# Kernel optimization log

Hardware: AMD Instinct MI355X
Metric: run time of the kernel (lower is better)

## Reference

```python
import jax, jax.numpy as jnp
import numpy as np

B, T, IN, H, LAYERS = 32, 512, 512, 512, 2


def _lstm_dir(x, Wx, Wh, b, reverse):
    """AugmentedLstm with highway, one direction.
    x: (B,T,I), Wx: (I,6H), Wh: (H,5H), b: (5H). Returns (B,T,H), h_final, c_final."""
    h = Wh.shape[0]
    # precompute input projections for all timesteps: (T,B,6H)
    px = jnp.einsum('bti,ig->tbg', x, Wx)
    if reverse:
        px = px[::-1]
    bsz = x.shape[0]
    h0 = jnp.zeros((bsz, h), x.dtype)
    c0 = jnp.zeros((bsz, h), x.dtype)

    def step(carry, pxt):
        hp, cp = carry
        ps = hp @ Wh + b  # (B,5H)
        i = jax.nn.sigmoid(pxt[:, 0*h:1*h] + ps[:, 0*h:1*h])
        f = jax.nn.sigmoid(pxt[:, 1*h:2*h] + ps[:, 1*h:2*h])
        g = jnp.tanh(pxt[:, 2*h:3*h] + ps[:, 2*h:3*h])
        o = jax.nn.sigmoid(pxt[:, 3*h:4*h] + ps[:, 3*h:4*h])
        c = i * g + f * cp
        ht = o * jnp.tanh(c)
        # highway: gate*h_t + (1-gate)*(W_x2 x_t)
        r = jax.nn.sigmoid(pxt[:, 4*h:5*h] + ps[:, 4*h:5*h])
        ht = r * ht + (1.0 - r) * pxt[:, 5*h:6*h]
        return (ht, c), ht

    (hf, cf), ys = jax.lax.scan(step, (h0, c0), px)
    if reverse:
        ys = ys[::-1]
    return jnp.transpose(ys, (1, 0, 2)), hf, cf


def setup_inputs() -> dict:
    key = jax.random.key(0)
    ks = jax.random.split(key, 16)
    d = {'x': jax.random.normal(ks[0], (B, T, IN), jnp.float32)}
    in_sizes = [IN, 2 * H]
    i = 1
    for l in range(LAYERS):
        isz = in_sizes[l]
        for dname in ('f', 'b'):
            d[f'Wx{l}{dname}'] = jax.random.normal(ks[i], (isz, 6 * H), jnp.float32) / np.sqrt(isz); i += 1
            d[f'Wh{l}{dname}'] = jax.random.normal(ks[i], (H, 5 * H), jnp.float32) / np.sqrt(H); i += 1
            d[f'b{l}{dname}'] = jnp.zeros((5 * H,), jnp.float32)
    return d


def reference(x, Wx0f, Wh0f, b0f, Wx0b, Wh0b, b0b,
              Wx1f, Wh1f, b1f, Wx1b, Wh1b, b1b):
    params = [((Wx0f, Wh0f, b0f), (Wx0b, Wh0b, b0b)),
              ((Wx1f, Wh1f, b1f), (Wx1b, Wh1b, b1b))]
    out = x
    final_h, final_c = [], []
    for (pf, pb) in params:
        yf, hf, cf = _lstm_dir(out, *pf, reverse=False)
        yb, hb, cb = _lstm_dir(out, *pb, reverse=True)
        out = jnp.concatenate([yf, yb], axis=-1)  # (B,T,2H)
        final_h.append(jnp.concatenate([hf, hb], axis=-1)[None])  # (1,B,2H)
        final_c.append(jnp.concatenate([cf, cb], axis=-1)[None])
    # torch code cats per-layer (1,B,2H) states along dim=1 -> (1, layers*B, 2H)
    final_h = jnp.concatenate(final_h, axis=1)
    final_c = jnp.concatenate(final_c, axis=1)
    return out, final_h, final_c
```

## Files before the change

### kernel.cpp

```cpp
#include <hip/hip_runtime.h>


typedef float f32x4 __attribute__((ext_vector_type(4)));
typedef __bf16 bf16x8 __attribute__((ext_vector_type(8)));
typedef unsigned short us8 __attribute__((ext_vector_type(8)));
typedef unsigned short us4 __attribute__((ext_vector_type(4)));
typedef unsigned int u32x4 __attribute__((ext_vector_type(4)));

__device__ __forceinline__ unsigned short f2bf(float f) {
  unsigned int u = __float_as_uint(f);
  u += 0x7FFFu + ((u >> 16) & 1u);
  return (unsigned short)(u >> 16);
}
__device__ __forceinline__ float bf2f(unsigned short h) {
  return __uint_as_float(((unsigned int)h) << 16);
}
__device__ __forceinline__ float sigf(float x) { return 1.0f / (1.0f + __expf(-x)); }
__device__ __forceinline__ float tanh_(float x) { return 2.0f / (1.0f + __expf(-2.0f * x)) - 1.0f; }

#define MFMA(a, b, c) __builtin_amdgcn_mfma_f32_16x16x32_bf16((a), (b), (c), 0, 0, 0)
#define GLOAD_LDS(gp, lp)                                                           \
  __builtin_amdgcn_global_load_lds(                                                 \
      (const __attribute__((address_space(1))) void*)(gp),                          \
      (__attribute__((address_space(3))) void*)(lp), 16, 0, 0)

__device__ __forceinline__ void chunk2_load(const char* p, u32x4& a, u32x4& b) {
  asm volatile(
      "global_load_dwordx4 %0, %2, off sc0 sc1\n\t"
      "global_load_dwordx4 %1, %2, off offset:16 sc0 sc1"
      : "=&v"(a), "=&v"(b) : "v"(p) : "memory");
}
__device__ __forceinline__ void hstore16(char* p, u32x4 v) {
  asm volatile("global_store_dwordx4 %0, %1, off sc0 sc1" :: "v"(p), "v"(v) : "memory");
}


__global__ void k_convert_x(const float* __restrict__ x, unsigned short* __restrict__ xb, int n4) {
  int i = blockIdx.x * blockDim.x + threadIdx.x;
  if (i < n4) {
    float4 v = ((const float4*)x)[i];
    us4 o;
    o[0] = f2bf(v.x); o[1] = f2bf(v.y); o[2] = f2bf(v.z); o[3] = f2bf(v.w);
    ((us4*)xb)[i] = o;
  }
}

__global__ __launch_bounds__(256) void k_pack_wxT(
    const float* __restrict__ W0, const float* __restrict__ W1,
    const float* __restrict__ W2, const float* __restrict__ W3,
    unsigned short* __restrict__ o01, unsigned short* __restrict__ o23) {
  int y = blockIdx.z;
  int K = (y >> 1) ? 1024 : 512;
  int kb = blockIdx.y * 32;
  if (kb >= K) return;
  const float* W = (y == 0) ? W0 : (y == 1) ? W1 : (y == 2) ? W2 : W3;
  unsigned short* o = (y >> 1) ? (o23 + (size_t)(y & 1) * 3072 * 1024)
                               : (o01 + (size_t)(y & 1) * 3072 * 512);
  __shared__ float tile[32][33];
  int nb = blockIdx.x * 32;
  int tx = threadIdx.x & 31, ty = threadIdx.x >> 5;
#pragma unroll
  for (int r = 0; r < 4; ++r)
    tile[ty + r * 8][tx] = W[(size_t)(kb + ty + r * 8) * 3072 + nb + tx];
  __syncthreads();
#pragma unroll
  for (int r = 0; r < 4; ++r)
    o[(size_t)(nb + ty + r * 8) * K + kb + tx] = f2bf(tile[tx][ty + r * 8]);
}

__global__ void k_pack_whp(const float* __restrict__ W0, const float* __restrict__ W1,
                           const float* __restrict__ W2, const float* __restrict__ W3,
                           unsigned short* __restrict__ out) {
  int y = blockIdx.y;
  const float* W = (y == 0) ? W0 : (y == 1) ? W1 : (y == 2) ? W2 : W3;
  unsigned short* o = out + (size_t)y * 1310720;
  int v = blockIdx.x * 256 + threadIdx.x;
  int lane = v & 63, ks = (v >> 6) & 15, ns = (v >> 10) & 31, g = v >> 15;
  int col = g * 512 + ns * 16 + (lane & 15);
  int kb = ks * 32 + ((lane >> 4) << 3);
  us8 vec;
#pragma unroll
  for (int e = 0; e < 8; ++e) vec[e] = f2bf(W[(size_t)(kb + e) * 2560 + col]);
  *(us8*)&o[(size_t)v * 8] = vec;
}

__global__ __launch_bounds__(256) void k_gemm(const unsigned short* __restrict__ A,
                                              const unsigned short* __restrict__ BtBase,
                                              unsigned short* __restrict__ CBase, int K) {
  __shared__ __align__(128) unsigned short As[128 * 32];
  __shared__ __align__(128) unsigned short Bs[128 * 32];
  const unsigned short* Bt = BtBase + (size_t)blockIdx.z * 3072 * K;
  unsigned short* C = CBase + (size_t)blockIdx.z * 16384 * 3072;
  int tid = threadIdx.x;
  int w = tid >> 6, l = tid & 63;
  int m0 = blockIdx.x * 128, n0 = blockIdx.y * 128;
  int wr = (w >> 1) * 64, wc = (w & 1) * 64;
  f32x4 acc[4][4];
#pragma unroll
  for (int i = 0; i < 4; ++i)
#pragma unroll
    for (int j = 0; j < 4; ++j) acc[i][j] = (f32x4){0.f, 0.f, 0.f, 0.f};

  for (int k0 = 0; k0 < K; k0 += 32) {
    __syncthreads();
#pragma unroll
    for (int half = 0; half < 2; ++half) {
      int r = w * 32 + half * 16 + (l >> 2);
      int gq = (l & 3) ^ (r & 3);
      GLOAD_LDS(A + (size_t)(m0 + r) * K + k0 + gq * 8, &As[(w * 32 + half * 16) * 32]);
      GLOAD_LDS(Bt + (size_t)(n0 + r) * K + k0 + gq * 8, &Bs[(w * 32 + half * 16) * 32]);
    }
    __syncthreads();
    bf16x8 af[4], bfr[4];
#pragma unroll
    for (int mi = 0; mi < 4; ++mi) {
      int r = wr + mi * 16 + (l & 15);
      int q = (l >> 4) ^ (r & 3);
      af[mi] = __builtin_bit_cast(bf16x8, *(const us8*)&As[r * 32 + q * 8]);
    }
#pragma unroll
    for (int ni = 0; ni < 4; ++ni) {
      int r = wc + ni * 16 + (l & 15);
      int q = (l >> 4) ^ (r & 3);
      bfr[ni] = __builtin_bit_cast(bf16x8, *(const us8*)&Bs[r * 32 + q * 8]);
    }
#pragma unroll
    for (int mi = 0; mi < 4; ++mi)
#pragma unroll
      for (int ni = 0; ni < 4; ++ni) acc[mi][ni] = MFMA(af[mi], bfr[ni], acc[mi][ni]);
  }
#pragma unroll
  for (int mi = 0; mi < 4; ++mi)
#pragma unroll
    for (int ni = 0; ni < 4; ++ni)
#pragma unroll
      for (int r4 = 0; r4 < 4; ++r4) {
        int row = m0 + wr + mi * 16 + (l >> 4) * 4 + r4;
        int rr = ((row & 511) << 5) + (row >> 9);
        int col = n0 + wc + ni * 16 + (l & 15);
        C[(size_t)rr * 3072 + col] = f2bf(acc[mi][ni][r4]);
      }
}

__global__ __launch_bounds__(256, 1) void k_persist(
    const unsigned short* __restrict__ px,
    const unsigned short* __restrict__ wp,
    const float* __restrict__ bias_f, const float* __restrict__ bias_b,
    char* __restrict__ hxc,
    unsigned short* __restrict__ ybf,
    float* __restrict__ yf,
    float* __restrict__ finals,
    int layer) {
  __shared__ float part[4][8][80];
  int wg = blockIdx.x;
  int grp = wg >> 4, m = wg & 15;
  int d = grp & 1, q = grp >> 1;
  int tid = threadIdx.x;
  int w = tid >> 6, l = tid & 63;
  int kh = w >> 1, nh = w & 1;
  int ns = m * 2 + nh;
  const unsigned short* wpd = wp + (size_t)d * 1310720;
  const unsigned short* pxd = px + (size_t)d * 16384 * 3072;
  const float* bias = d ? bias_b : bias_f;

  bf16x8 wf[5][8];
#pragma unroll
  for (int g5 = 0; g5 < 5; ++g5)
#pragma unroll
    for (int kk = 0; kk < 8; ++kk)
      wf[g5][kk] = __builtin_bit_cast(
          bf16x8,
          *(const us8*)&wpd[(size_t)((g5 * 32 + ns) * 16 + kh * 8 + kk) * 512 + l * 8]);

  int r = tid >> 5, j = tid & 31, jg = m * 32 + j, b = q * 8 + r;
  float bv[5];
#pragma unroll
  for (int g5 = 0; g5 < 5; ++g5) bv[g5] = bias[(g5 << 9) + jg];

  float c = 0.f;
  unsigned short xv[6];
  {
    int t0 = d ? 511 : 0;
    const unsigned short* pp = pxd + ((size_t)((t0 << 5) + b)) * 3072 + jg;
#pragma unroll
    for (int q6 = 0; q6 < 6; ++q6) xv[q6] = pp[q6 << 9];
  }

  int sel = l >> 4;
  int p0 = (sel == 1) ? 1 : (sel == 2) ? 2 : (sel == 3) ? 4 : 0;
  bool s1 = (sel == 1), s2 = (sel == 2);
  int lrow = l & 15;
  int row8 = l & 7;
  char* hxg = hxc + (size_t)grp * 12288;
  int coff[8];
#pragma unroll
  for (int kk = 0; kk < 8; ++kk)
    coff[kk] = (((kh * 8 + kk) * 8 + row8) * 6 + p0) * 16;
  int myc = l & 31;
  int pbase = l & 32;
  int prow = 2 * w + (l >> 5);

  for (int s = 0; s < 512; ++s) {
    int t = d ? (511 - s) : s;
    char* cbase = hxg + (size_t)(s & 1) * 98304;

    u32x4 ca[8], cb2[8];
    {
      unsigned int tgt = (unsigned int)s;
      long guard = 0;
      bool ok;
      do {
        if (lrow < 8) {
#pragma unroll
          for (int kk = 0; kk < 8; ++kk)
            chunk2_load(cbase + coff[kk], ca[kk], cb2[kk]);
        }
        asm volatile("s_waitcnt vmcnt(0)" ::: "memory");
        bool mine = true;
        if (lrow < 8) {
#pragma unroll
          for (int kk = 0; kk < 8; ++kk)
            mine = mine && (ca[kk][3] == tgt) && (cb2[kk][3] == tgt);
        }
        ok = (__all((int)mine) != 0);
      } while (!ok && ++guard < 50000);
    }

    f32x4 acc[5];
#pragma unroll
    for (int g5 = 0; g5 < 5; ++g5) acc[g5] = (f32x4){0.f, 0.f, 0.f, 0.f};
#pragma unroll
    for (int kk = 0; kk < 8; ++kk) {
      u32x4 a = ca[kk], bb = cb2[kk], f;
      f[0] = s1 ? a[1] : (s2 ? a[2] : a[0]);
      f[1] = s1 ? a[2] : (s2 ? bb[0] : a[1]);
      f[2] = s1 ? bb[0] : (s2 ? bb[1] : a[2]);
      f[3] = s1 ? bb[1] : (s2 ? bb[2] : bb[0]);
      bf16x8 av = __builtin_bit_cast(bf16x8, f);
#pragma unroll
      for (int g5 = 0; g5 < 5; ++g5) acc[g5] = MFMA(av, wf[g5][kk], acc[g5]);
    }
    if (l < 32) {
#pragma unroll
      for (int g5 = 0; g5 < 5; ++g5)
#pragma unroll
        for (int r4 = 0; r4 < 4; ++r4)
          part[w][(l >> 4) * 4 + r4][g5 * 16 + (l & 15)] = acc[g5][r4];
    }
    __syncthreads();

    float ht;
    {
      int nhe = j >> 4, jc = j & 15;
      float ps_[5];
#pragma unroll
      for (int g5 = 0; g5 < 5; ++g5) {
        int cc = g5 * 16 + jc;
        ps_[g5] = part[nhe][r][cc] + part[2 + nhe][r][cc] + bv[g5];
      }
      float x0 = bf2f(xv[0]), x1 = bf2f(xv[1]), x2 = bf2f(xv[2]);
      float x3 = bf2f(xv[3]), x4 = bf2f(xv[4]), x5 = bf2f(xv[5]);
      float iG = sigf(x0 + ps_[0]);
      float fG = sigf(x1 + ps_[1]);
      float gG = tanh_(x2 + ps_[2]);
      float oG = sigf(x3 + ps_[3]);
      float cn = iG * gG + fG * c;
      c = cn;
      ht = oG * tanh_(cn);
      float rG = sigf(x4 + ps_[4]);
      ht = rG * ht + (1.f - rG) * x5;
      size_t yo = ((size_t)(b * 512 + t)) * 1024 + d * 512 + jg;
      if (ybf) ybf[yo] = f2bf(ht);
      else     yf[yo] = ht;
      if (s == 511) {
        int fo = (layer * 32 + b) * 1024 + d * 512 + jg;
        finals[fo] = ht;
        finals[65536 + fo] = cn;
      }
    }

    if (s < 511) {
      unsigned int hbits = (unsigned int)f2bf(ht);
      unsigned int vv[6];
#pragma unroll
      for (int i = 0; i < 6; ++i)
        vv[i] = __shfl(hbits, (pbase + myc * 6 + i) & 63);
      unsigned int pw0 = vv[0] | (vv[1] << 16);
      unsigned int pw1 = vv[2] | (vv[3] << 16);
      unsigned int pw2 = vv[4] | (vv[5] << 16);
      if (myc == 5) { pw1 = 0; pw2 = 0; }
      if (myc < 6) {
        char* dst = hxg + (size_t)((s + 1) & 1) * 98304 +
                    (size_t)(((m * 8 + prow) * 6 + myc)) * 16;
        u32x4 pv = {pw0, pw1, pw2, (unsigned int)(s + 1)};
        hstore16(dst, pv);
      }
      int tn = d ? (511 - (s + 1)) : (s + 1);
      const unsigned short* pp = pxd + ((size_t)((tn << 5) + b)) * 3072 + jg;
#pragma unroll
      for (int q6 = 0; q6 < 6; ++q6) xv[q6] = pp[q6 << 9];
    }
    __syncthreads();
  }
}


extern "C" void kernel_launch(void* const* d_in, const int* in_sizes, int n_in,
                              void* d_out, int out_size, void* d_ws, size_t ws_size,
                              hipStream_t stream) {
  (void)in_sizes; (void)n_in; (void)out_size; (void)ws_size;
  const float* x = (const float*)d_in[0];
  const float* Wx[4] = {(const float*)d_in[1], (const float*)d_in[4],
                        (const float*)d_in[7], (const float*)d_in[10]};
  const float* Wh[4] = {(const float*)d_in[2], (const float*)d_in[5],
                        (const float*)d_in[8], (const float*)d_in[11]};
  const float* bs[4] = {(const float*)d_in[3], (const float*)d_in[6],
                        (const float*)d_in[9], (const float*)d_in[12]};

  char* ws = (char*)d_ws;
  unsigned short* px   = (unsigned short*)(ws);
  unsigned short* whp  = (unsigned short*)(ws + 201326592);
  char*           hxc  = (char*)(ws + 211812352);

  char* ob = (char*)d_out;
  unsigned short* xbf  = (unsigned short*)(ob);
  unsigned short* wxt0 = (unsigned short*)(ob + 16777216);
  unsigned short* wxt1 = (unsigned short*)(ob + 33554432);
  unsigned short* a1bf = (unsigned short*)(ob);
  float* out = (float*)d_out;
  float* finals = out + 16777216;

  k_convert_x<<<8192, 256, 0, stream>>>(x, xbf, 2097152);
  k_pack_wxT<<<dim3(96, 32, 4), 256, 0, stream>>>(Wx[0], Wx[1], Wx[2], Wx[3], wxt0, wxt1);
  k_pack_whp<<<dim3(640, 4), 256, 0, stream>>>(Wh[0], Wh[1], Wh[2], Wh[3], whp);

  for (int layer = 0; layer < 2; ++layer) {
    int K = layer ? 1024 : 512;
    const unsigned short* Ag = layer ? a1bf : xbf;
    const unsigned short* wxt = layer ? wxt1 : wxt0;
    k_gemm<<<dim3(128, 24, 2), 256, 0, stream>>>(Ag, wxt, px, K);
    hipMemsetAsync(hxc, 0, 196608, stream);
    k_persist<<<128, 256, 0, stream>>>(
        px, whp + (size_t)layer * 2621440, bs[layer * 2], bs[layer * 2 + 1],
        hxc, layer ? nullptr : a1bf, layer ? out : nullptr, finals, layer);
  }
}
```

Baseline: 3.111 ms.

## Split recurrent K across 8 waves, double-buffer partials, drop second barrier

```diff
diff --git a/kernel.cpp b/kernel.cpp
--- a/kernel.cpp
+++ b/kernel.cpp
@@ -12,8 +12,8 @@
   u += 0x7FFFu + ((u >> 16) & 1u);
   return (unsigned short)(u >> 16);
 }
-__device__ __forceinline__ float bf2f(unsigned short h) {
-  return __uint_as_float(((unsigned int)h) << 16);
+__device__ __forceinline__ float bf2f(unsigned int h) {
+  return __uint_as_float(h << 16);
 }
 __device__ __forceinline__ float sigf(float x) { return 1.0f / (1.0f + __expf(-x)); }
 __device__ __forceinline__ float tanh_(float x) { return 2.0f / (1.0f + __expf(-2.0f * x)) - 1.0f; }
@@ -24,13 +24,12 @@
       (const __attribute__((address_space(1))) void*)(gp),                          \
       (__attribute__((address_space(3))) void*)(lp), 16, 0, 0)
 
-__device__ __forceinline__ void chunk2_load(const char* p, u32x4& a, u32x4& b) {
-  asm volatile(
-      "global_load_dwordx4 %0, %2, off sc0 sc1\n\t"
-      "global_load_dwordx4 %1, %2, off offset:16 sc0 sc1"
-      : "=&v"(a), "=&v"(b) : "v"(p) : "memory");
-}
-__device__ __forceinline__ void hstore16(char* p, u32x4 v) {
+__device__ __forceinline__ void chunk2_ld(const char* p, u32x4& a, u32x4& b) {
+  asm volatile("global_load_dwordx4 %0, %2, off sc0 sc1\n\t"
+               "global_load_dwordx4 %1, %2, off offset:16 sc0 sc1"
+               : "=&v"(a), "=&v"(b) : "v"(p) : "memory");
+}
+__device__ __forceinline__ void pub16(char* p, u32x4 v) {
   asm volatile("global_store_dwordx4 %0, %1, off sc0 sc1" :: "v"(p), "v"(v) : "memory");
 }
 
@@ -84,6 +83,8 @@
   *(us8*)&o[(size_t)v * 8] = vec;
 }
 
+__device__ __forceinline__ unsigned short f2bf(float f);
+
 __global__ __launch_bounds__(256) void k_gemm(const unsigned short* __restrict__ A,
                                               const unsigned short* __restrict__ BtBase,
                                               unsigned short* __restrict__ CBase, int K) {
@@ -142,7 +143,7 @@
       }
 }
 
-__global__ __launch_bounds__(256, 1) void k_persist(
+__global__ __launch_bounds__(512, 1) void k_persist(
     const unsigned short* __restrict__ px,
     const unsigned short* __restrict__ wp,
     const float* __restrict__ bias_f, const float* __restrict__ bias_b,
@@ -151,124 +152,156 @@
     float* __restrict__ yf,
     float* __restrict__ finals,
     int layer) {
-  __shared__ float part[4][8][80];
+  __shared__ float part[2][4][8][160];
   int wg = blockIdx.x;
   int grp = wg >> 4, m = wg & 15;
   int d = grp & 1, q = grp >> 1;
   int tid = threadIdx.x;
   int w = tid >> 6, l = tid & 63;
-  int kh = w >> 1, nh = w & 1;
+  int kh = w & 3, nh = w >> 2;
   int ns = m * 2 + nh;
   const unsigned short* wpd = wp + (size_t)d * 1310720;
   const unsigned short* pxd = px + (size_t)d * 16384 * 3072;
   const float* bias = d ? bias_b : bias_f;
-
-  bf16x8 wf[5][8];
+  char* hxg = hxc + (size_t)layer * 196608 + (size_t)grp * 12288;
+
+  bf16x8 wf[5][4];
 #pragma unroll
   for (int g5 = 0; g5 < 5; ++g5)
 #pragma unroll
-    for (int kk = 0; kk < 8; ++kk)
+    for (int kk = 0; kk < 4; ++kk)
       wf[g5][kk] = __builtin_bit_cast(
           bf16x8,
-          *(const us8*)&wpd[(size_t)((g5 * 32 + ns) * 16 + kh * 8 + kk) * 512 + l * 8]);
-
+          *(const us8*)&wpd[(size_t)((g5 * 32 + ns) * 16 + (kh * 4 + kk)) * 512 + l * 8]);
+
+  bool epi = tid < 256;
   int r = tid >> 5, j = tid & 31, jg = m * 32 + j, b = q * 8 + r;
   float bv[5];
 #pragma unroll
   for (int g5 = 0; g5 < 5; ++g5) bv[g5] = bias[(g5 << 9) + jg];
 
   float c = 0.f;
-  unsigned short xv[6];
-  {
+  unsigned int xCur[6], xNext[6];
+  if (epi) {
     int t0 = d ? 511 : 0;
     const unsigned short* pp = pxd + ((size_t)((t0 << 5) + b)) * 3072 + jg;
 #pragma unroll
-    for (int q6 = 0; q6 < 6; ++q6) xv[q6] = pp[q6 << 9];
-  }
-
+    for (int q6 = 0; q6 < 6; ++q6) xNext[q6] = pp[q6 << 9];
+  }
+
+  bool lrow8 = (l & 15) < 8;
+  int row8 = l & 7;
   int sel = l >> 4;
   int p0 = (sel == 1) ? 1 : (sel == 2) ? 2 : (sel == 3) ? 4 : 0;
   bool s1 = (sel == 1), s2 = (sel == 2);
-  int lrow = l & 15;
-  int row8 = l & 7;
-  char* hxg = hxc + (size_t)grp * 12288;
-  int coff[8];
-#pragma unroll
-  for (int kk = 0; kk < 8; ++kk)
-    coff[kk] = (((kh * 8 + kk) * 8 + row8) * 6 + p0) * 16;
-  int myc = l & 31;
-  int pbase = l & 32;
-  int prow = 2 * w + (l >> 5);
+  int coff[4];
+#pragma unroll
+  for (int kk = 0; kk < 4; ++kk)
+    coff[kk] = (((kh * 4 + kk) * 8 + row8) * 6 + p0) * 16;
+  int myc = l & 31, pbase = l & 32, prow = 2 * w + (l >> 5);
 
   for (int s = 0; s < 512; ++s) {
     int t = d ? (511 - s) : s;
-    char* cbase = hxg + (size_t)(s & 1) * 98304;
-
-    u32x4 ca[8], cb2[8];
-    {
-      unsigned int tgt = (unsigned int)s;
+    u32x4 ca[4], cb2[4];
+
+    if (s > 0) {
+      const char* cb = hxg + (size_t)(s & 1) * 98304;
+      unsigned enc = (unsigned)(s | ((~s & 0xFFFF) << 16));
       long guard = 0;
       bool ok;
       do {
-        if (lrow < 8) {
-#pragma unroll
-          for (int kk = 0; kk < 8; ++kk)
-            chunk2_load(cbase + coff[kk], ca[kk], cb2[kk]);
+        if (lrow8) {
+#pragma unroll
+          for (int kk = 0; kk < 4; ++kk) chunk2_ld(cb + coff[kk], ca[kk], cb2[kk]);
         }
         asm volatile("s_waitcnt vmcnt(0)" ::: "memory");
+        __builtin_amdgcn_sched_barrier(0);
         bool mine = true;
-        if (lrow < 8) {
-#pragma unroll
-          for (int kk = 0; kk < 8; ++kk)
-            mine = mine && (ca[kk][3] == tgt) && (cb2[kk][3] == tgt);
+        if (lrow8) {
+#pragma unroll
+          for (int kk = 0; kk < 4; ++kk)
+            mine = mine && (ca[kk][3] == enc) && (cb2[kk][3] == enc);
         }
         ok = (__all((int)mine) != 0);
-      } while (!ok && ++guard < 50000);
+      } while (!ok && ++guard < 300000L);
+    }
+
+    if (epi) {
+#pragma unroll
+      for (int i = 0; i < 6; ++i) xCur[i] = xNext[i];
+      if (s < 511) {
+        int tn = d ? (511 - (s + 1)) : (s + 1);
+        const unsigned short* pp = pxd + ((size_t)((tn << 5) + b)) * 3072 + jg;
+#pragma unroll
+        for (int q6 = 0; q6 < 6; ++q6) xNext[q6] = pp[q6 << 9];
+      }
     }
 
     f32x4 acc[5];
 #pragma unroll
     for (int g5 = 0; g5 < 5; ++g5) acc[g5] = (f32x4){0.f, 0.f, 0.f, 0.f};
-#pragma unroll
-    for (int kk = 0; kk < 8; ++kk) {
-      u32x4 a = ca[kk], bb = cb2[kk], f;
-      f[0] = s1 ? a[1] : (s2 ? a[2] : a[0]);
-      f[1] = s1 ? a[2] : (s2 ? bb[0] : a[1]);
-      f[2] = s1 ? bb[0] : (s2 ? bb[1] : a[2]);
-      f[3] = s1 ? bb[1] : (s2 ? bb[2] : bb[0]);
-      bf16x8 av = __builtin_bit_cast(bf16x8, f);
-#pragma unroll
-      for (int g5 = 0; g5 < 5; ++g5) acc[g5] = MFMA(av, wf[g5][kk], acc[g5]);
+    if (s > 0) {
+#pragma unroll
+      for (int kk = 0; kk < 4; ++kk) {
+        u32x4 a = ca[kk], bb = cb2[kk], f;
+        f[0] = s1 ? a[1] : (s2 ? a[2] : a[0]);
+        f[1] = s1 ? a[2] : (s2 ? bb[0] : a[1]);
+        f[2] = s1 ? bb[0] : (s2 ? bb[1] : a[2]);
+        f[3] = s1 ? bb[1] : (s2 ? bb[2] : bb[0]);
+        bf16x8 av = __builtin_bit_cast(bf16x8, f);
+#pragma unroll
+        for (int g5 = 0; g5 < 5; ++g5) acc[g5] = MFMA(av, wf[g5][kk], acc[g5]);
+      }
     }
     if (l < 32) {
 #pragma unroll
       for (int g5 = 0; g5 < 5; ++g5)
 #pragma unroll
         for (int r4 = 0; r4 < 4; ++r4)
-          part[w][(l >> 4) * 4 + r4][g5 * 16 + (l & 15)] = acc[g5][r4];
+          part[s & 1][kh][(l >> 4) * 4 + r4][nh * 80 + g5 * 16 + (l & 15)] = acc[g5][r4];
     }
     __syncthreads();
 
-    float ht;
-    {
-      int nhe = j >> 4, jc = j & 15;
+    if (epi) {
+      int cc0 = (j >> 4) * 80 + (j & 15);
       float ps_[5];
 #pragma unroll
       for (int g5 = 0; g5 < 5; ++g5) {
-        int cc = g5 * 16 + jc;
-        ps_[g5] = part[nhe][r][cc] + part[2 + nhe][r][cc] + bv[g5];
-      }
-      float x0 = bf2f(xv[0]), x1 = bf2f(xv[1]), x2 = bf2f(xv[2]);
-      float x3 = bf2f(xv[3]), x4 = bf2f(xv[4]), x5 = bf2f(xv[5]);
+        int cc = cc0 + g5 * 16;
+        ps_[g5] = part[s & 1][0][r][cc] + part[s & 1][1][r][cc] +
+                  part[s & 1][2][r][cc] + part[s & 1][3][r][cc] + bv[g5];
+      }
+      float x0 = bf2f(xCur[0]), x1 = bf2f(xCur[1]), x2 = bf2f(xCur[2]);
+      float x3 = bf2f(xCur[3]), x4 = bf2f(xCur[4]), x5 = bf2f(xCur[5]);
       float iG = sigf(x0 + ps_[0]);
       float fG = sigf(x1 + ps_[1]);
       float gG = tanh_(x2 + ps_[2]);
       float oG = sigf(x3 + ps_[3]);
       float cn = iG * gG + fG * c;
       c = cn;
-      ht = oG * tanh_(cn);
+      float ht = oG * tanh_(cn);
       float rG = sigf(x4 + ps_[4]);
       ht = rG * ht + (1.f - rG) * x5;
+
+      if (s < 511) {
+        unsigned int hbits = (unsigned int)f2bf(ht);
+        unsigned int vv[6];
+#pragma unroll
+        for (int i = 0; i < 6; ++i)
+          vv[i] = __shfl(hbits, (pbase + myc * 6 + i) & 63);
+        unsigned int pw0 = vv[0] | (vv[1] << 16);
+        unsigned int pw1 = vv[2] | (vv[3] << 16);
+        unsigned int pw2 = vv[4] | (vv[5] << 16);
+        if (myc == 5) { pw1 = 0; pw2 = 0; }
+        if (myc < 6) {
+          char* dst = hxg + (size_t)((s + 1) & 1) * 98304 +
+                      (size_t)((m * 8 + prow) * 6 + myc) * 16;
+          unsigned enc1 = (unsigned)((s + 1) | ((~(s + 1) & 0xFFFF) << 16));
+          u32x4 pv = {pw0, pw1, pw2, enc1};
+          pub16(dst, pv);
+        }
+      }
+
       size_t yo = ((size_t)(b * 512 + t)) * 1024 + d * 512 + jg;
       if (ybf) ybf[yo] = f2bf(ht);
       else     yf[yo] = ht;
@@ -278,29 +311,6 @@
         finals[65536 + fo] = cn;
       }
     }
-
-    if (s < 511) {
-      unsigned int hbits = (unsigned int)f2bf(ht);
-      unsigned int vv[6];
-#pragma unroll
-      for (int i = 0; i < 6; ++i)
-        vv[i] = __shfl(hbits, (pbase + myc * 6 + i) & 63);
-      unsigned int pw0 = vv[0] | (vv[1] << 16);
-      unsigned int pw1 = vv[2] | (vv[3] << 16);
-      unsigned int pw2 = vv[4] | (vv[5] << 16);
-      if (myc == 5) { pw1 = 0; pw2 = 0; }
-      if (myc < 6) {
-        char* dst = hxg + (size_t)((s + 1) & 1) * 98304 +
-                    (size_t)(((m * 8 + prow) * 6 + myc)) * 16;
-        u32x4 pv = {pw0, pw1, pw2, (unsigned int)(s + 1)};
-        hstore16(dst, pv);
-      }
-      int tn = d ? (511 - (s + 1)) : (s + 1);
-      const unsigned short* pp = pxd + ((size_t)((tn << 5) + b)) * 3072 + jg;
-#pragma unroll
-      for (int q6 = 0; q6 < 6; ++q6) xv[q6] = pp[q6 << 9];
-    }
-    __syncthreads();
   }
 }
 
@@ -333,14 +343,14 @@
   k_convert_x<<<8192, 256, 0, stream>>>(x, xbf, 2097152);
   k_pack_wxT<<<dim3(96, 32, 4), 256, 0, stream>>>(Wx[0], Wx[1], Wx[2], Wx[3], wxt0, wxt1);
   k_pack_whp<<<dim3(640, 4), 256, 0, stream>>>(Wh[0], Wh[1], Wh[2], Wh[3], whp);
+  hipMemsetAsync(hxc, 0xFF, 393216, stream);
 
   for (int layer = 0; layer < 2; ++layer) {
     int K = layer ? 1024 : 512;
     const unsigned short* Ag = layer ? a1bf : xbf;
     const unsigned short* wxt = layer ? wxt1 : wxt0;
     k_gemm<<<dim3(128, 24, 2), 256, 0, stream>>>(Ag, wxt, px, K);
-    hipMemsetAsync(hxc, 0, 196608, stream);
-    k_persist<<<128, 256, 0, stream>>>(
+    k_persist<<<128, 512, 0, stream>>>(
         px, whp + (size_t)layer * 2621440, bs[layer * 2], bs[layer * 2 + 1],
         hxc, layer ? nullptr : a1bf, layer ? out : nullptr, finals, layer);
   }
```

Result: slower. 3.339 ms (+7.3%).
